# Kernel tuning notes

Measured on AMD Instinct MI355X. Metric: run time of the kernel, lower is better.

The kernel has to match this reference:

```python
import jax, jax.numpy as jnp
import numpy as np

IN_FEATURES = 4096
OUT_FEATURES = 11008
W_BITS = 4
GROUP_SIZE = 128
NUM_CHERRIES = 128                       # ceil(4096*0.03125)//8*8
NUM_NORMAL = IN_FEATURES - NUM_CHERRIES  # 3968
N_GROUPS = NUM_NORMAL // GROUP_SIZE      # 31
QROWS = NUM_NORMAL // 8 * W_BITS         # 1984 packed uint8 rows
QMIN = -(2 ** (W_BITS - 1))              # signed int4 min = -8
BATCH = 64


def setup_inputs() -> dict:
    key = jax.random.key(0)
    k1, k2, k3, k4, k5 = jax.random.split(key, 5)
    x = jax.random.normal(k1, (BATCH, IN_FEATURES), jnp.float32)
    # packed 4-bit weights: two nibbles per uint8, stored as [QROWS, out]
    qweight = jax.random.randint(k2, (QROWS, OUT_FEATURES), 0, 256, jnp.int32).astype(jnp.uint8)
    # per-group scales, stored transposed as [n_groups, out]
    scales = jax.random.uniform(k3, (N_GROUPS, OUT_FEATURES), jnp.float32, 0.005, 0.02)
    # full-precision outlier ('cherry') columns, stored as [num_cherries, out]
    cherry_weight = jax.random.normal(k4, (NUM_CHERRIES, OUT_FEATURES), jnp.float32) * 0.02
    rng = np.random.default_rng(0)
    cherry_indices = jnp.asarray(
        np.sort(rng.choice(IN_FEATURES, NUM_CHERRIES, replace=False)).astype(np.int32))
    bias = jax.random.normal(k5, (OUT_FEATURES,), jnp.float32) * 0.01
    return {"x": x, "qweight": qweight, "cherry_weight": cherry_weight,
            "cherry_indices": cherry_indices, "scales": scales, "bias": bias}


def _normal_indices(cherry_indices):
    # complement of cherry_indices, as in the torch scatter/nonzero construction
    mask = jnp.ones((IN_FEATURES,), dtype=bool).at[cherry_indices].set(False)
    return jnp.nonzero(mask, size=NUM_NORMAL)[0]  # static size -> jit ok


def reference(x, qweight, cherry_weight, cherry_indices, scales, bias):
    # --- unpack 4-bit weights (matches QuantLinear.unpack for w_bits=4) ---
    q = qweight.T                                    # [out, QROWS]
    nib = jnp.stack([q & 0xF, (q >> 4) & 0xF], axis=-1)  # low nibble first
    nib = nib.reshape(OUT_FEATURES, NUM_NORMAL)
    intw = nib.astype(jnp.int32) + QMIN              # signed int4 values
    # --- dequantize: repeat-interleave per-group scales along in dim ---
    s = jnp.repeat(scales.T, GROUP_SIZE, axis=1)     # [out, NUM_NORMAL]
    w_normal = intw.astype(s.dtype) * s              # dequantized normal weight
    # --- merge cherry outlier columns via column-gather on x (same math as
    #     scattering into a full [out, in] weight then x @ W.T) ---
    normal_idx = _normal_indices(cherry_indices)
    out = x[:, normal_idx] @ w_normal.T + x[:, cherry_indices] @ cherry_weight
    return out + bias
```

## Files before the change

kernel.cpp:

```cpp
#include <hip/hip_runtime.h>
#include <hip/hip_bf16.h>
#include <stdint.h>

#define IN_F 4096
#define OUT_F 11008
#define NUM_CH 128
#define NUM_NORM 3968
#define BATCH 64
#define KSPLIT 16
#define KCHUNK (IN_F / KSPLIT)
#define NMEGA 2
#define BS 136

typedef short short8 __attribute__((ext_vector_type(8)));
typedef float float4v __attribute__((ext_vector_type(4)));
typedef int int4v __attribute__((ext_vector_type(4)));

__device__ __forceinline__ void barrier_no_vmcnt() {
    asm volatile("s_waitcnt lgkmcnt(0)\n\ts_barrier" ::: "memory");
}

__device__ __forceinline__ unsigned short f2bf(float f) {
    union { float f; unsigned u; } v; v.f = f;
    unsigned u = v.u;
    return (unsigned short)((u + 0x7FFFu + ((u >> 16) & 1u)) >> 16);
}

__device__ __forceinline__ unsigned pk_bf16(float lo, float hi) {
    __hip_bfloat162 h = __float22bfloat162_rn(make_float2(lo, hi));
    union { __hip_bfloat162 h; unsigned u; } c; c.h = h; return c.u;
}

__global__ __launch_bounds__(256) void permute_x(
        const float* __restrict__ x, const int* __restrict__ cidx,
        unsigned short* __restrict__ xp) {
    int i = blockIdx.x * blockDim.x + threadIdx.x;
    int b = blockIdx.y;
    int lo = 0, hi = NUM_CH;
    while (lo < hi) { int mid = (lo + hi) >> 1; if (cidx[mid] < i) lo = mid + 1; else hi = mid; }
    bool isch = (lo < NUM_CH) && (cidx[lo] == i);
    int pos = isch ? (NUM_NORM + lo) : (i - lo);
    xp[b * IN_F + pos] = f2bf(x[b * IN_F + i]);
}

__global__ __launch_bounds__(256) void reduce_out(
        const float* __restrict__ part, const float* __restrict__ bias,
        float* __restrict__ out) {
    const int i = blockIdx.x * 256 + threadIdx.x;
    const int c = i % (OUT_F / 4);
    float4v s = *reinterpret_cast<const float4v*>(bias + c * 4);
    #pragma unroll
    for (int ky = 0; ky < KSPLIT; ++ky) {
        const float4v p = reinterpret_cast<const float4v*>(
            part + (size_t)ky * BATCH * OUT_F)[i];
        s = (float4v){s[0] + p[0], s[1] + p[1], s[2] + p[2], s[3] + p[3]};
    }
    reinterpret_cast<float4v*>(out)[i] = s;
}

__global__ __launch_bounds__(256, 2) void qgemm(
        const unsigned short* __restrict__ xp, const int* __restrict__ qw,
        const float* __restrict__ cw, const float* __restrict__ scales,
        float* __restrict__ part) {
    __shared__ unsigned short Bt[2][64][BS];

    const int tid  = threadIdx.x;
    const int wave = tid >> 6;
    const int lane = tid & 63;
    const int ln   = lane & 15;
    const int lq   = lane >> 4;
    const int n0    = blockIdx.x * 64;
    const int ky    = blockIdx.y;
    const int kbase = ky * KCHUNK;
    const int tcol = (tid & 15) << 2;
    const int trow = tid >> 4;

    const int*   qbase = qw + n0 + tcol;
    const float* sbase = scales + n0 + tcol;
    const float* cbase = cw + n0 + tcol;

    short8 a_all[4][8];
    #pragma unroll
    for (int mt = 0; mt < 4; ++mt) {
        const unsigned short* ap = xp + (size_t)(mt * 16 + ln) * IN_F + kbase + (lq << 3);
        #pragma unroll
        for (int j = 0; j < 8; ++j)
            a_all[mt][j] = *reinterpret_cast<const short8*>(ap + j * 32);
    }
    int4v qc[4];
    {
        const int rb = (kbase >> 1) + 4 * trow;
        #pragma unroll
        for (int i = 0; i < 4; ++i)
            qc[i] = *reinterpret_cast<const int4v*>(qbase + (size_t)(rb + i) * OUT_F);
    }
    float4v sc0 = *reinterpret_cast<const float4v*>(
        sbase + (size_t)(kbase >> 7) * OUT_F);
    float4v sc1 = sc0;
    const bool m1_normal = (kbase + 128 < NUM_NORM);
    if (m1_normal)
        sc1 = *reinterpret_cast<const float4v*>(
            sbase + (size_t)((kbase >> 7) + 1) * OUT_F);

    float4v acc[4];
    #pragma unroll
    for (int s = 0; s < 4; ++s) acc[s] = (float4v){0.f, 0.f, 0.f, 0.f};

    #pragma unroll
    for (int s = 0; s < NMEGA; ++s) {
        const int k0 = kbase + s * 128;
        unsigned short (*buf)[BS] = Bt[s];

        if (s == 0 || m1_normal) {
            const int4v q0 = qc[0], q1 = qc[1], q2 = qc[2], q3 = qc[3];
            const float4v sc = (s == 0) ? sc0 : sc1;
            if (s == 0 && m1_normal) {
                const int rb = ((k0 + 128) >> 1) + 4 * trow;
                #pragma unroll
                for (int i = 0; i < 4; ++i)
                    qc[i] = *reinterpret_cast<const int4v*>(qbase + (size_t)(rb + i) * OUT_F);
            }
            const int4v qq[4] = {q0, q1, q2, q3};
            #pragma unroll
            for (int cc = 0; cc < 4; ++cc) {
                union { short8 v; unsigned u[4]; } wv;
                const float s1 = sc[cc];
                #pragma unroll
                for (int i = 0; i < 4; ++i) {
                    const int q = qq[i][cc];
                    wv.u[i] = pk_bf16((float)((q & 0xF) - 8) * s1,
                                      (float)(((q >> 4) & 0xF) - 8) * s1);
                }
                *reinterpret_cast<short8*>(&buf[tcol + cc][trow * 8]) = wv.v;
            }
        } else {
            float4v ch[8];
            #pragma unroll
            for (int j = 0; j < 8; ++j)
                ch[j] = *reinterpret_cast<const float4v*>(
                    cbase + (size_t)(8 * trow + j) * OUT_F);
            #pragma unroll
            for (int cc = 0; cc < 4; ++cc) {
                union { short8 v; unsigned u[4]; } wv;
                #pragma unroll
                for (int m = 0; m < 4; ++m)
                    wv.u[m] = pk_bf16(ch[2 * m][cc], ch[2 * m + 1][cc]);
                *reinterpret_cast<short8*>(&buf[tcol + cc][trow * 8]) = wv.v;
            }
        }

        barrier_no_vmcnt();

        const unsigned short* brow = &buf[(wave << 4) + ln][lq << 3];
        const short8 b0 = *reinterpret_cast<const short8*>(brow);
        const short8 b1 = *reinterpret_cast<const short8*>(brow + 32);
        const short8 b2 = *reinterpret_cast<const short8*>(brow + 64);
        const short8 b3 = *reinterpret_cast<const short8*>(brow + 96);

        #pragma unroll
        for (int mt = 0; mt < 4; ++mt) {
            acc[mt] = __builtin_amdgcn_mfma_f32_16x16x32_bf16(a_all[mt][s * 4 + 0], b0, acc[mt], 0, 0, 0);
            acc[mt] = __builtin_amdgcn_mfma_f32_16x16x32_bf16(a_all[mt][s * 4 + 1], b1, acc[mt], 0, 0, 0);
            acc[mt] = __builtin_amdgcn_mfma_f32_16x16x32_bf16(a_all[mt][s * 4 + 2], b2, acc[mt], 0, 0, 0);
            acc[mt] = __builtin_amdgcn_mfma_f32_16x16x32_bf16(a_all[mt][s * 4 + 3], b3, acc[mt], 0, 0, 0);
        }
    }

    float* pbase = part + (size_t)blockIdx.y * BATCH * OUT_F;
    const int n = n0 + (wave << 4) + ln;
    #pragma unroll
    for (int mt = 0; mt < 4; ++mt) {
        #pragma unroll
        for (int r = 0; r < 4; ++r) {
            const int m = mt * 16 + (lq << 2) + r;
            pbase[(size_t)m * OUT_F + n] = acc[mt][r];
        }
    }
}

extern "C" void kernel_launch(void* const* d_in, const int* in_sizes, int n_in,
                              void* d_out, int out_size, void* d_ws, size_t ws_size,
                              hipStream_t stream) {
    const float* x      = (const float*)d_in[0];
    const int*   qw     = (const int*)d_in[1];
    const float* cw     = (const float*)d_in[2];
    const int*   cidx   = (const int*)d_in[3];
    const float* scales = (const float*)d_in[4];
    const float* bias   = (const float*)d_in[5];
    float*       out    = (float*)d_out;

    unsigned short* xp   = (unsigned short*)d_ws;
    float*          part = (float*)((char*)d_ws + (512 << 10));

    dim3 pgrid(IN_F / 256, BATCH);
    permute_x<<<pgrid, 256, 0, stream>>>(x, cidx, xp);
    qgemm<<<dim3(OUT_F / 64, KSPLIT), 256, 0, stream>>>(xp, qw, cw, scales, part);
    reduce_out<<<(BATCH * OUT_F / 4) / 256, 256, 0, stream>>>(part, bias, out);
}
```

Baseline: 184.6 us.

## Widen N tile to 256 with 32-wide K substeps and swizzled LDS

The GEMM block now covers 256 output columns instead of 64, walking its 256-element K chunk in eight 32-wide sub-steps with a double-buffered LDS tile. The LDS row index is XOR-swizzled to avoid bank conflicts. Activation fragments are prefetched one step ahead instead of all being held in registers. This reuses each A fragment across four N fragments to cut redundant activation loads, but it drops the grid to 43x16 blocks, removes the launch_bounds occupancy hint, and adds eight barriers per block.

```diff
diff --git a/kernel.cpp b/kernel.cpp
--- a/kernel.cpp
+++ b/kernel.cpp
@@ -8,9 +8,10 @@
 #define NUM_NORM 3968
 #define BATCH 64
 #define KSPLIT 16
-#define KCHUNK (IN_F / KSPLIT)
-#define NMEGA 2
-#define BS 136
+#define KCHUNK 256
+#define NSUB 8
+#define NTILE 256
+#define BS 40
 
 typedef short short8 __attribute__((ext_vector_type(8)));
 typedef float float4v __attribute__((ext_vector_type(4)));
@@ -58,71 +59,71 @@
     reinterpret_cast<float4v*>(out)[i] = s;
 }
 
-__global__ __launch_bounds__(256, 2) void qgemm(
+__global__ void qgemm(
         const unsigned short* __restrict__ xp, const int* __restrict__ qw,
         const float* __restrict__ cw, const float* __restrict__ scales,
         float* __restrict__ part) {
-    __shared__ unsigned short Bt[2][64][BS];
+    __shared__ unsigned short Bt[2][NTILE][BS];
 
     const int tid  = threadIdx.x;
     const int wave = tid >> 6;
     const int lane = tid & 63;
     const int ln   = lane & 15;
     const int lq   = lane >> 4;
-    const int n0    = blockIdx.x * 64;
+    const int n0    = blockIdx.x * NTILE;
     const int ky    = blockIdx.y;
     const int kbase = ky * KCHUNK;
-    const int tcol = (tid & 15) << 2;
-    const int trow = tid >> 4;
-
-    const int*   qbase = qw + n0 + tcol;
-    const float* sbase = scales + n0 + tcol;
-    const float* cbase = cw + n0 + tcol;
-
-    short8 a_all[4][8];
-    #pragma unroll
-    for (int mt = 0; mt < 4; ++mt) {
-        const unsigned short* ap = xp + (size_t)(mt * 16 + ln) * IN_F + kbase + (lq << 3);
-        #pragma unroll
-        for (int j = 0; j < 8; ++j)
-            a_all[mt][j] = *reinterpret_cast<const short8*>(ap + j * 32);
-    }
+
+    const int nb = (tid & 63) << 2;
+    const int rg = tid >> 6;
+
+    const int*   qbase = qw + n0 + nb;
+    const float* sbase = scales + n0 + nb;
+    const float* cbase = cw + n0 + nb;
+
+    float4v scg[2];
+    scg[0] = *reinterpret_cast<const float4v*>(sbase + (size_t)(2 * ky) * OUT_F);
+    scg[1] = (2 * ky + 1 <= 30)
+        ? *reinterpret_cast<const float4v*>(sbase + (size_t)(2 * ky + 1) * OUT_F)
+        : scg[0];
+
+    float4v acc[4][4];
+    #pragma unroll
+    for (int a = 0; a < 4; ++a)
+        #pragma unroll
+        for (int b = 0; b < 4; ++b) acc[a][b] = (float4v){0.f, 0.f, 0.f, 0.f};
+
     int4v qc[4];
     {
-        const int rb = (kbase >> 1) + 4 * trow;
+        const size_t rb = (size_t)(kbase >> 1) + 4 * rg;
         #pragma unroll
         for (int i = 0; i < 4; ++i)
-            qc[i] = *reinterpret_cast<const int4v*>(qbase + (size_t)(rb + i) * OUT_F);
-    }
-    float4v sc0 = *reinterpret_cast<const float4v*>(
-        sbase + (size_t)(kbase >> 7) * OUT_F);
-    float4v sc1 = sc0;
-    const bool m1_normal = (kbase + 128 < NUM_NORM);
-    if (m1_normal)
-        sc1 = *reinterpret_cast<const float4v*>(
-            sbase + (size_t)((kbase >> 7) + 1) * OUT_F);
-
-    float4v acc[4];
-    #pragma unroll
-    for (int s = 0; s < 4; ++s) acc[s] = (float4v){0.f, 0.f, 0.f, 0.f};
-
-    #pragma unroll
-    for (int s = 0; s < NMEGA; ++s) {
-        const int k0 = kbase + s * 128;
-        unsigned short (*buf)[BS] = Bt[s];
-
-        if (s == 0 || m1_normal) {
+            qc[i] = *reinterpret_cast<const int4v*>(qbase + (rb + i) * OUT_F);
+    }
+    short8 acur[4];
+    #pragma unroll
+    for (int mt = 0; mt < 4; ++mt)
+        acur[mt] = *reinterpret_cast<const short8*>(
+            xp + (size_t)(mt * 16 + ln) * IN_F + kbase + (lq << 3));
+
+    for (int s = 0; s < NSUB; ++s) {
+        const int k0 = kbase + 32 * s;
+        unsigned short (*buf)[BS] = Bt[s & 1];
+        const bool normal = (k0 < NUM_NORM);
+
+        if (normal) {
             const int4v q0 = qc[0], q1 = qc[1], q2 = qc[2], q3 = qc[3];
-            const float4v sc = (s == 0) ? sc0 : sc1;
-            if (s == 0 && m1_normal) {
-                const int rb = ((k0 + 128) >> 1) + 4 * trow;
+            const float4v sc = scg[s >> 2];
+            if (s + 1 < NSUB && k0 + 32 < NUM_NORM) {
+                const size_t rb = (size_t)((k0 + 32) >> 1) + 4 * rg;
                 #pragma unroll
                 for (int i = 0; i < 4; ++i)
-                    qc[i] = *reinterpret_cast<const int4v*>(qbase + (size_t)(rb + i) * OUT_F);
+                    qc[i] = *reinterpret_cast<const int4v*>(qbase + (rb + i) * OUT_F);
             }
             const int4v qq[4] = {q0, q1, q2, q3};
             #pragma unroll
             for (int cc = 0; cc < 4; ++cc) {
+                const int n = nb + cc;
                 union { short8 v; unsigned u[4]; } wv;
                 const float s1 = sc[cc];
                 #pragma unroll
@@ -131,49 +132,66 @@
                     wv.u[i] = pk_bf16((float)((q & 0xF) - 8) * s1,
                                       (float)(((q >> 4) & 0xF) - 8) * s1);
                 }
-                *reinterpret_cast<short8*>(&buf[tcol + cc][trow * 8]) = wv.v;
+                const int gp = rg ^ ((n >> 2) & 3);
+                *reinterpret_cast<short8*>(&buf[n][gp << 3]) = wv.v;
             }
         } else {
-            float4v ch[8];
-            #pragma unroll
-            for (int j = 0; j < 8; ++j)
-                ch[j] = *reinterpret_cast<const float4v*>(
-                    cbase + (size_t)(8 * trow + j) * OUT_F);
-            #pragma unroll
-            for (int cc = 0; cc < 4; ++cc) {
-                union { short8 v; unsigned u[4]; } wv;
+            const int crow0 = 32 * s - 128;
+            #pragma unroll
+            for (int j = 0; j < 8; ++j) {
+                const int kl = 8 * rg + j;
+                const float4v ch = *reinterpret_cast<const float4v*>(
+                    cbase + (size_t)(crow0 + kl) * OUT_F);
                 #pragma unroll
-                for (int m = 0; m < 4; ++m)
-                    wv.u[m] = pk_bf16(ch[2 * m][cc], ch[2 * m + 1][cc]);
-                *reinterpret_cast<short8*>(&buf[tcol + cc][trow * 8]) = wv.v;
-            }
+                for (int i = 0; i < 4; ++i) {
+                    const int n = nb + i;
+                    const int g = kl >> 3, go = kl & 7;
+                    const int gp = g ^ ((n >> 2) & 3);
+                    buf[n][(gp << 3) + go] = f2bf(ch[i]);
+                }
+            }
+        }
+        short8 anxt[4];
+        if (s + 1 < NSUB) {
+            #pragma unroll
+            for (int mt = 0; mt < 4; ++mt)
+                anxt[mt] = *reinterpret_cast<const short8*>(
+                    xp + (size_t)(mt * 16 + ln) * IN_F + k0 + 32 + (lq << 3));
         }
 
         barrier_no_vmcnt();
 
-        const unsigned short* brow = &buf[(wave << 4) + ln][lq << 3];
-        const short8 b0 = *reinterpret_cast<const short8*>(brow);
-        const short8 b1 = *reinterpret_cast<const short8*>(brow + 32);
-        const short8 b2 = *reinterpret_cast<const short8*>(brow + 64);
-        const short8 b3 = *reinterpret_cast<const short8*>(brow + 96);
-
-        #pragma unroll
-        for (int mt = 0; mt < 4; ++mt) {
-            acc[mt] = __builtin_amdgcn_mfma_f32_16x16x32_bf16(a_all[mt][s * 4 + 0], b0, acc[mt], 0, 0, 0);
-            acc[mt] = __builtin_amdgcn_mfma_f32_16x16x32_bf16(a_all[mt][s * 4 + 1], b1, acc[mt], 0, 0, 0);
-            acc[mt] = __builtin_amdgcn_mfma_f32_16x16x32_bf16(a_all[mt][s * 4 + 2], b2, acc[mt], 0, 0, 0);
-            acc[mt] = __builtin_amdgcn_mfma_f32_16x16x32_bf16(a_all[mt][s * 4 + 3], b3, acc[mt], 0, 0, 0);
-        }
-    }
-
-    float* pbase = part + (size_t)blockIdx.y * BATCH * OUT_F;
-    const int n = n0 + (wave << 4) + ln;
+        short8 bf[4];
+        #pragma unroll
+        for (int nf = 0; nf < 4; ++nf) {
+            const int n = nf * 64 + (wave << 4) + ln;
+            const int gp = lq ^ ((n >> 2) & 3);
+            bf[nf] = *reinterpret_cast<const short8*>(&buf[n][gp << 3]);
+        }
+        #pragma unroll
+        for (int mt = 0; mt < 4; ++mt)
+            #pragma unroll
+            for (int nf = 0; nf < 4; ++nf)
+                acc[mt][nf] = __builtin_amdgcn_mfma_f32_16x16x32_bf16(
+                    acur[mt], bf[nf], acc[mt][nf], 0, 0, 0);
+
+        if (s + 1 < NSUB) {
+            #pragma unroll
+            for (int mt = 0; mt < 4; ++mt) acur[mt] = anxt[mt];
+        }
+    }
+
+    float* pbase = part + (size_t)ky * BATCH * OUT_F;
     #pragma unroll
     for (int mt = 0; mt < 4; ++mt) {
         #pragma unroll
-        for (int r = 0; r < 4; ++r) {
-            const int m = mt * 16 + (lq << 2) + r;
-            pbase[(size_t)m * OUT_F + n] = acc[mt][r];
+        for (int nf = 0; nf < 4; ++nf) {
+            const int n = n0 + nf * 64 + (wave << 4) + ln;
+            #pragma unroll
+            for (int r = 0; r < 4; ++r) {
+                const int m = mt * 16 + (lq << 2) + r;
+                pbase[(size_t)m * OUT_F + n] = acc[mt][nf][r];
+            }
         }
     }
 }
@@ -194,6 +212,6 @@
 
     dim3 pgrid(IN_F / 256, BATCH);
     permute_x<<<pgrid, 256, 0, stream>>>(x, cidx, xp);
-    qgemm<<<dim3(OUT_F / 64, KSPLIT), 256, 0, stream>>>(xp, qw, cw, scales, part);
+    qgemm<<<dim3(OUT_F / NTILE, KSPLIT), 256, 0, stream>>>(xp, qw, cw, scales, part);
     reduce_out<<<(BATCH * OUT_F / 4) / 256, 256, 0, stream>>>(part, bias, out);
 }
```

Result: slower. 217.9 us (+18.0%).
